# Kernel tuning notes

Hardware: AMD Instinct MI355X
Metric: run time of the kernel (lower is better)

Reference implementation:

```python
import jax, jax.numpy as jnp
import numpy as np

IMG_H = 1080
IMG_W = 1440
LAMBDA_REG = 0.01


def setup_inputs() -> dict:
    key = jax.random.key(0)
    k1, k2, k3, k4 = jax.random.split(key, 4)
    B, N = 64, 100000
    return {
        "img_points": jax.random.normal(k1, (B, N, 2), dtype=jnp.float32),
        "projected_lid_points": jax.random.normal(k2, (B, N, 2), dtype=jnp.float32),
        "mat_reg_loss": jax.random.uniform(k3, (B,), dtype=jnp.float32),
        "lid_cents_proj_Org": jax.random.normal(k4, (B, N, 2), dtype=jnp.float32),
    }


def reference(img_points, projected_lid_points, mat_reg_loss, lid_cents_proj_Org):
    denom = jnp.float32(max(IMG_H, IMG_W))
    # per-batch mean euclidean distance between point sets, shape [B]
    batch_loss = jnp.mean(
        jnp.linalg.norm(projected_lid_points - img_points, axis=-1), axis=-1) / denom
    batch_loss_org = jnp.mean(
        jnp.linalg.norm(lid_cents_proj_Org - img_points, axis=-1), axis=-1) / denom
    diff = batch_loss - batch_loss_org  # [B]
    reward = (1.0 + 5.0 * jax.nn.relu(-diff)) * diff
    penalty = 5.0 * jax.nn.relu(diff)
    per_batch_final = (reward + penalty) / (1.0 + jnp.abs(diff))
    # total_loss_final = 1000 * sum_b(...) / B  == 1000 * mean
    return 1000.0 * jnp.mean(per_batch_final)
```

## Files before the change

kernel.cpp:

```cpp
#include <hip/hip_runtime.h>


#define ML_B 64
#define ML_N 100000
#define ML_DENOM 1440.0f
#define ML_F4_PER_BATCH (ML_N * 2 / 4)
#define ML_BLOCKS_PER_BATCH 32
#define ML_BLOCK 256

__global__ __launch_bounds__(ML_BLOCK) void ml_partial_kernel(
    const float4* __restrict__ img,
    const float4* __restrict__ plid,
    const float4* __restrict__ org,
    float* __restrict__ ws)
{
    const int b   = blockIdx.x >> 5;
    const int blk = blockIdx.x & 31;
    const long base = (long)b * ML_F4_PER_BATCH;

    float acc = 0.0f;
    const int stride = ML_BLOCKS_PER_BATCH * ML_BLOCK;
    for (int i = blk * ML_BLOCK + threadIdx.x; i < ML_F4_PER_BATCH; i += stride) {
        float4 a = img[base + i];
        float4 p = plid[base + i];
        float4 o = org[base + i];
        float dx1 = p.x - a.x, dy1 = p.y - a.y;
        float dx2 = p.z - a.z, dy2 = p.w - a.w;
        float ex1 = o.x - a.x, ey1 = o.y - a.y;
        float ex2 = o.z - a.z, ey2 = o.w - a.w;
        acc += sqrtf(dx1 * dx1 + dy1 * dy1) - sqrtf(ex1 * ex1 + ey1 * ey1);
        acc += sqrtf(dx2 * dx2 + dy2 * dy2) - sqrtf(ex2 * ex2 + ey2 * ey2);
    }

    #pragma unroll
    for (int off = 32; off > 0; off >>= 1)
        acc += __shfl_down(acc, off, 64);

    __shared__ float sdata[ML_BLOCK / 64];
    const int lane = threadIdx.x & 63;
    const int wave = threadIdx.x >> 6;
    if (lane == 0) sdata[wave] = acc;
    __syncthreads();
    if (threadIdx.x == 0) {
        float s = sdata[0] + sdata[1] + sdata[2] + sdata[3];
        atomicAdd(&ws[b], s);
    }
}

__global__ void ml_final_kernel(const float* __restrict__ ws,
                                float* __restrict__ out)
{
    const int b = threadIdx.x;
    float s = ws[b];
    float diff = s * (1.0f / ((float)ML_N * ML_DENOM));
    float reward  = (1.0f + 5.0f * fmaxf(-diff, 0.0f)) * diff;
    float penalty = 5.0f * fmaxf(diff, 0.0f);
    float v = (reward + penalty) / (1.0f + fabsf(diff));

    #pragma unroll
    for (int off = 32; off > 0; off >>= 1)
        v += __shfl_down(v, off, 64);

    if (b == 0) out[0] = 1000.0f * v * (1.0f / (float)ML_B);
}

extern "C" void kernel_launch(void* const* d_in, const int* in_sizes, int n_in,
                              void* d_out, int out_size, void* d_ws, size_t ws_size,
                              hipStream_t stream) {
    const float4* img  = (const float4*)d_in[0];
    const float4* plid = (const float4*)d_in[1];
    const float4* org  = (const float4*)d_in[3];
    float* ws  = (float*)d_ws;
    float* out = (float*)d_out;

    hipMemsetAsync(ws, 0, ML_B * sizeof(float), stream);

    ml_partial_kernel<<<ML_B * ML_BLOCKS_PER_BATCH, ML_BLOCK, 0, stream>>>(
        img, plid, org, ws);
    ml_final_kernel<<<1, 64, 0, stream>>>(ws, out);
}
```

Before: 171.5 us.

## Unroll loads for more memory parallelism, drop memset and atomics via per-block partials

Halves blocks per batch and fully unrolls the strided loop so each thread issues twelve independent float4 loads per group of four iterations, plus a tail. Per-block partial sums are written directly to the workspace instead of being atomically added, which removes the memset launch. The final kernel now reduces 1024 partials in two stages. This trades a larger final reduction and higher register use for fewer launches and more loads in flight in the bandwidth-bound pass.

```diff
diff --git a/kernel.cpp b/kernel.cpp
--- a/kernel.cpp
+++ b/kernel.cpp
@@ -5,8 +5,20 @@
 #define ML_N 100000
 #define ML_DENOM 1440.0f
 #define ML_F4_PER_BATCH (ML_N * 2 / 4)
-#define ML_BLOCKS_PER_BATCH 32
+#define ML_BPB 16
 #define ML_BLOCK 256
+#define ML_TPB (ML_BPB * ML_BLOCK)
+#define ML_FULL_K 12
+#define ML_TAIL (ML_F4_PER_BATCH - ML_FULL_K * ML_TPB)
+
+__device__ inline float pair_term(float4 a, float4 p, float4 o) {
+    float dx1 = p.x - a.x, dy1 = p.y - a.y;
+    float dx2 = p.z - a.z, dy2 = p.w - a.w;
+    float ex1 = o.x - a.x, ey1 = o.y - a.y;
+    float ex2 = o.z - a.z, ey2 = o.w - a.w;
+    return sqrtf(dx1 * dx1 + dy1 * dy1) - sqrtf(ex1 * ex1 + ey1 * ey1)
+         + sqrtf(dx2 * dx2 + dy2 * dy2) - sqrtf(ex2 * ex2 + ey2 * ey2);
+}
 
 __global__ __launch_bounds__(ML_BLOCK) void ml_partial_kernel(
     const float4* __restrict__ img,
@@ -14,22 +26,38 @@
     const float4* __restrict__ org,
     float* __restrict__ ws)
 {
-    const int b   = blockIdx.x >> 5;
-    const int blk = blockIdx.x & 31;
+    const int b   = blockIdx.x >> 4;
+    const int blk = blockIdx.x & 15;
     const long base = (long)b * ML_F4_PER_BATCH;
+    const int pos = blk * ML_BLOCK + threadIdx.x;
+
+    const float4* __restrict__ ib = img  + base;
+    const float4* __restrict__ pb = plid + base;
+    const float4* __restrict__ ob = org  + base;
 
     float acc = 0.0f;
-    const int stride = ML_BLOCKS_PER_BATCH * ML_BLOCK;
-    for (int i = blk * ML_BLOCK + threadIdx.x; i < ML_F4_PER_BATCH; i += stride) {
-        float4 a = img[base + i];
-        float4 p = plid[base + i];
-        float4 o = org[base + i];
-        float dx1 = p.x - a.x, dy1 = p.y - a.y;
-        float dx2 = p.z - a.z, dy2 = p.w - a.w;
-        float ex1 = o.x - a.x, ey1 = o.y - a.y;
-        float ex2 = o.z - a.z, ey2 = o.w - a.w;
-        acc += sqrtf(dx1 * dx1 + dy1 * dy1) - sqrtf(ex1 * ex1 + ey1 * ey1);
-        acc += sqrtf(dx2 * dx2 + dy2 * dy2) - sqrtf(ex2 * ex2 + ey2 * ey2);
+    #pragma unroll
+    for (int k = 0; k < ML_FULL_K; k += 4) {
+        float4 a0 = ib[pos + (k + 0) * ML_TPB];
+        float4 a1 = ib[pos + (k + 1) * ML_TPB];
+        float4 a2 = ib[pos + (k + 2) * ML_TPB];
+        float4 a3 = ib[pos + (k + 3) * ML_TPB];
+        float4 p0 = pb[pos + (k + 0) * ML_TPB];
+        float4 p1 = pb[pos + (k + 1) * ML_TPB];
+        float4 p2 = pb[pos + (k + 2) * ML_TPB];
+        float4 p3 = pb[pos + (k + 3) * ML_TPB];
+        float4 o0 = ob[pos + (k + 0) * ML_TPB];
+        float4 o1 = ob[pos + (k + 1) * ML_TPB];
+        float4 o2 = ob[pos + (k + 2) * ML_TPB];
+        float4 o3 = ob[pos + (k + 3) * ML_TPB];
+        acc += pair_term(a0, p0, o0);
+        acc += pair_term(a1, p1, o1);
+        acc += pair_term(a2, p2, o2);
+        acc += pair_term(a3, p3, o3);
+    }
+    if (pos < ML_TAIL) {
+        const int idx = ML_FULL_K * ML_TPB + pos;
+        acc += pair_term(ib[idx], pb[idx], ob[idx]);
     }
 
     #pragma unroll
@@ -41,27 +69,43 @@
     const int wave = threadIdx.x >> 6;
     if (lane == 0) sdata[wave] = acc;
     __syncthreads();
-    if (threadIdx.x == 0) {
-        float s = sdata[0] + sdata[1] + sdata[2] + sdata[3];
-        atomicAdd(&ws[b], s);
-    }
+    if (threadIdx.x == 0)
+        ws[blockIdx.x] = sdata[0] + sdata[1] + sdata[2] + sdata[3];
 }
 
-__global__ void ml_final_kernel(const float* __restrict__ ws,
-                                float* __restrict__ out)
+__global__ __launch_bounds__(1024) void ml_final_kernel(
+    const float* __restrict__ ws, float* __restrict__ out)
 {
-    const int b = threadIdx.x;
-    float s = ws[b];
-    float diff = s * (1.0f / ((float)ML_N * ML_DENOM));
-    float reward  = (1.0f + 5.0f * fmaxf(-diff, 0.0f)) * diff;
-    float penalty = 5.0f * fmaxf(diff, 0.0f);
-    float v = (reward + penalty) / (1.0f + fabsf(diff));
+    const int t = threadIdx.x;
+    float v = ws[t];
+    v += __shfl_down(v, 8, 16);
+    v += __shfl_down(v, 4, 16);
+    v += __shfl_down(v, 2, 16);
+    v += __shfl_down(v, 1, 16);
+
+    float f = 0.0f;
+    if ((t & 15) == 0) {
+        float diff = v * (1.0f / ((float)ML_N * ML_DENOM));
+        float reward  = (1.0f + 5.0f * fmaxf(-diff, 0.0f)) * diff;
+        float penalty = 5.0f * fmaxf(diff, 0.0f);
+        f = (reward + penalty) / (1.0f + fabsf(diff));
+    }
 
     #pragma unroll
     for (int off = 32; off > 0; off >>= 1)
-        v += __shfl_down(v, off, 64);
+        f += __shfl_down(f, off, 64);
 
-    if (b == 0) out[0] = 1000.0f * v * (1.0f / (float)ML_B);
+    __shared__ float s[16];
+    if ((t & 63) == 0) s[t >> 6] = f;
+    __syncthreads();
+    if (t < 16) {
+        float x = s[t];
+        x += __shfl_down(x, 8, 16);
+        x += __shfl_down(x, 4, 16);
+        x += __shfl_down(x, 2, 16);
+        x += __shfl_down(x, 1, 16);
+        if (t == 0) out[0] = (1000.0f / (float)ML_B) * x;
+    }
 }
 
 extern "C" void kernel_launch(void* const* d_in, const int* in_sizes, int n_in,
@@ -73,9 +117,6 @@
     float* ws  = (float*)d_ws;
     float* out = (float*)d_out;
 
-    hipMemsetAsync(ws, 0, ML_B * sizeof(float), stream);
-
-    ml_partial_kernel<<<ML_B * ML_BLOCKS_PER_BATCH, ML_BLOCK, 0, stream>>>(
-        img, plid, org, ws);
-    ml_final_kernel<<<1, 64, 0, stream>>>(ws, out);
+    ml_partial_kernel<<<ML_B * ML_BPB, ML_BLOCK, 0, stream>>>(img, plid, org, ws);
+    ml_final_kernel<<<1, 1024, 0, stream>>>(ws, out);
 }
```

Result: no change. 170.4 us (-0.7%).
